# Performance work log

Measured on AMD Instinct MI355X. Metric: run time of the kernel, lower is better.

## Reference

```python
import jax, jax.numpy as jnp
import numpy as np

B, OUT, IN = 128, 1024, 1024
MASK_DENSITY = 0.05  # ~51 connected variable nodes per check node


def setup_inputs() -> dict:
    key = jax.random.key(0)
    kx, km = jax.random.split(key)
    x = jax.random.normal(kx, (B, IN), dtype=jnp.float32)
    # sparse binary connectivity mask [out_features, in_features]
    layer_mask = (jax.random.uniform(km, (OUT, IN)) < MASK_DENSITY).astype(jnp.float32)
    return {"x": x, "layer_mask": layer_mask}


def reference(x, layer_mask):
    # x: [B, IN], layer_mask: [OUT, IN]
    # Vectorized form of: for each output i, product over nonzero entries of
    # x * layer_mask[i]; zero if the masked row is entirely zero.
    xm = x[:, None, :] * layer_mask[None, :, :]          # [B, OUT, IN]
    nz = xm != 0                                          # [B, OUT, IN]
    prod = jnp.prod(jnp.where(nz, xm, jnp.ones_like(xm)), axis=-1)  # [B, OUT]
    return jnp.where(nz.any(axis=-1), prod, jnp.zeros_like(prod))    # [B, OUT]
```

## Files before the change

### kernel.cpp

```cpp
#include <hip/hip_runtime.h>

#define B_SZ   128
#define OUT_SZ 1024
#define IN_SZ  1024
#define IDX_STRIDE 1024


__global__ __launch_bounds__(512) void prep(const float* __restrict__ x,
                                            const float* __restrict__ mask,
                                            float* __restrict__ xT,
                                            int* __restrict__ g_cnt,
                                            int* __restrict__ g_idx) {
    __shared__ int   s_idx[IN_SZ];
    __shared__ int   s_wsum[8];
    __shared__ float s_tile[32][33];

    const int t = threadIdx.x;

    if (blockIdx.x >= OUT_SZ) {
        const int tb = blockIdx.x - OUT_SZ;
        const int c0 = (tb & 31) * 32;
        const int r0 = (tb >> 5) * 32;
        const int tx = t & 31, ty = t >> 5;
#pragma unroll
        for (int j = ty; j < 32; j += 16)
            s_tile[j][tx] = x[(r0 + j) * IN_SZ + c0 + tx];
        __syncthreads();
#pragma unroll
        for (int j = ty; j < 32; j += 16)
            xT[(c0 + j) * B_SZ + r0 + tx] = s_tile[tx][j];
        return;
    }

    const int o    = blockIdx.x;
    const int lane = t & 63;
    const int wv   = t >> 6;

    const float2 m = *reinterpret_cast<const float2*>(mask + o * IN_SZ + t * 2);
    const bool nx = (m.x != 0.0f);
    const bool ny = (m.y != 0.0f);
    const unsigned long long bx = __ballot(nx);
    const unsigned long long by = __ballot(ny);
    const unsigned long long mlow = ((unsigned long long)1 << lane) - 1;
    int off = __popcll(bx & mlow) + __popcll(by & mlow);
    if (lane == 0) s_wsum[wv] = __popcll(bx) + __popcll(by);
    __syncthreads();

    int base = 0, cnt = 0;
#pragma unroll
    for (int i = 0; i < 8; ++i) {
        int v = s_wsum[i];
        if (i < wv) base += v;
        cnt += v;
    }
    off += base;
    if (nx) s_idx[off]      = t * 2;
    if (ny) s_idx[off + nx] = t * 2 + 1;
    __syncthreads();

    for (int k = t; k < cnt; k += 512) g_idx[o * IDX_STRIDE + k] = s_idx[k];
    if (t == 0) g_cnt[o] = cnt;
}

__global__ __launch_bounds__(512) void cn_gather(const float* __restrict__ xT,
                                                 const int* __restrict__ g_cnt,
                                                 const int* __restrict__ g_idx,
                                                 float* __restrict__ out) {
    __shared__ int   s_idx[IDX_STRIDE];
    __shared__ float s_part[4][B_SZ];
    __shared__ int   s_nz[4][B_SZ];

    const int o = blockIdx.x;
    const int t = threadIdx.x;
    const int cnt = g_cnt[o];

    for (int k = t; k < cnt; k += 512) s_idx[k] = g_idx[o * IDX_STRIDE + k];
    __syncthreads();

    const int b = t & 127;
    const int s = t >> 7;

    float p0 = 1.0f, p1 = 1.0f;
    int   a0 = 0,    a1 = 0;
    int k = s;
    for (; k + 4 < cnt; k += 8) {
        const float v0 = xT[s_idx[k]     * B_SZ + b];
        const float v1 = xT[s_idx[k + 4] * B_SZ + b];
        const bool n0 = (v0 != 0.0f), n1 = (v1 != 0.0f);
        p0 *= n0 ? v0 : 1.0f;  a0 |= n0;
        p1 *= n1 ? v1 : 1.0f;  a1 |= n1;
    }
    if (k < cnt) {
        const float v0 = xT[s_idx[k] * B_SZ + b];
        const bool n0 = (v0 != 0.0f);
        p0 *= n0 ? v0 : 1.0f;  a0 |= n0;
    }
    s_part[s][b] = p0 * p1;
    s_nz[s][b]   = a0 | a1;
    __syncthreads();

    if (t < B_SZ) {
        const float p = s_part[0][t] * s_part[1][t] * s_part[2][t] * s_part[3][t];
        const int   a = s_nz[0][t] | s_nz[1][t] | s_nz[2][t] | s_nz[3][t];
        out[t * OUT_SZ + o] = a ? p : 0.0f;
    }
}

extern "C" void kernel_launch(void* const* d_in, const int* in_sizes, int n_in,
                              void* d_out, int out_size, void* d_ws, size_t ws_size,
                              hipStream_t stream) {
    const float* x    = (const float*)d_in[0];
    const float* mask = (const float*)d_in[1];
    float*       out  = (float*)d_out;

    char* ws = (char*)d_ws;
    float* xT    = (float*)(ws);
    int*   g_cnt = (int*)(ws + (512 << 10));
    int*   g_idx = (int*)(ws + (1 << 20));

    prep<<<OUT_SZ + 128, 512, 0, stream>>>(x, mask, xT, g_cnt, g_idx);
    cn_gather<<<OUT_SZ, 512, 0, stream>>>(xT, g_cnt, g_idx, out);
}
```

Measured before the change: 15.43 us.

## Process two outputs per block with float4 gathers in cn_gather

Each cn_gather block now handles two output columns instead of one, halving the grid. Each thread loads a float4 covering four batch entries, and the 16 slices stride over the connected indices. A final reduce over 16 partials per output packs the nonzero flags into a 4-bit mask. The aim is fewer, wider gather instructions and more work per block, at the cost of fewer blocks for parallelism and a longer serial reduction over 16 partials.

```diff
diff --git a/kernel.cpp b/kernel.cpp
--- a/kernel.cpp
+++ b/kernel.cpp
@@ -4,6 +4,7 @@
 #define OUT_SZ 1024
 #define IN_SZ  1024
 #define IDX_STRIDE 1024
+#define OPB    2
 
 
 __global__ __launch_bounds__(512) void prep(const float* __restrict__ x,
@@ -66,43 +67,57 @@
                                                  const int* __restrict__ g_cnt,
                                                  const int* __restrict__ g_idx,
                                                  float* __restrict__ out) {
-    __shared__ int   s_idx[IDX_STRIDE];
-    __shared__ float s_part[4][B_SZ];
-    __shared__ int   s_nz[4][B_SZ];
+    __shared__ int    s_idx[OPB][IDX_STRIDE];
+    __shared__ float4 s_part[OPB][16][32];
+    __shared__ int    s_nzm[OPB][16][32];
 
-    const int o = blockIdx.x;
-    const int t = threadIdx.x;
-    const int cnt = g_cnt[o];
+    const int o0 = blockIdx.x * OPB;
+    const int t  = threadIdx.x;
 
-    for (int k = t; k < cnt; k += 512) s_idx[k] = g_idx[o * IDX_STRIDE + k];
+    int cnt[OPB];
+#pragma unroll
+    for (int j = 0; j < OPB; ++j) {
+        cnt[j] = g_cnt[o0 + j];
+        for (int k = t; k < cnt[j]; k += 512)
+            s_idx[j][k] = g_idx[(o0 + j) * IDX_STRIDE + k];
+    }
     __syncthreads();
 
-    const int b = t & 127;
-    const int s = t >> 7;
+    const int bg = t & 31;
+    const int s  = t >> 5;
+    const float4* xT4 = reinterpret_cast<const float4*>(xT);
 
-    float p0 = 1.0f, p1 = 1.0f;
-    int   a0 = 0,    a1 = 0;
-    int k = s;
-    for (; k + 4 < cnt; k += 8) {
-        const float v0 = xT[s_idx[k]     * B_SZ + b];
-        const float v1 = xT[s_idx[k + 4] * B_SZ + b];
-        const bool n0 = (v0 != 0.0f), n1 = (v1 != 0.0f);
-        p0 *= n0 ? v0 : 1.0f;  a0 |= n0;
-        p1 *= n1 ? v1 : 1.0f;  a1 |= n1;
+#pragma unroll
+    for (int j = 0; j < OPB; ++j) {
+        float px = 1.f, py = 1.f, pz = 1.f, pw = 1.f;
+        int m = 0;
+        for (int k = s; k < cnt[j]; k += 16) {
+            const float4 v = xT4[s_idx[j][k] * 32 + bg];
+            const bool ax = (v.x != 0.0f), ay = (v.y != 0.0f);
+            const bool az = (v.z != 0.0f), aw = (v.w != 0.0f);
+            px *= ax ? v.x : 1.f;  py *= ay ? v.y : 1.f;
+            pz *= az ? v.z : 1.f;  pw *= aw ? v.w : 1.f;
+            m |= (ax ? 1 : 0) | (ay ? 2 : 0) | (az ? 4 : 0) | (aw ? 8 : 0);
+        }
+        s_part[j][s][bg] = make_float4(px, py, pz, pw);
+        s_nzm[j][s][bg]  = m;
     }
-    if (k < cnt) {
-        const float v0 = xT[s_idx[k] * B_SZ + b];
-        const bool n0 = (v0 != 0.0f);
-        p0 *= n0 ? v0 : 1.0f;  a0 |= n0;
-    }
-    s_part[s][b] = p0 * p1;
-    s_nz[s][b]   = a0 | a1;
     __syncthreads();
 
-    if (t < B_SZ) {
-        const float p = s_part[0][t] * s_part[1][t] * s_part[2][t] * s_part[3][t];
-        const int   a = s_nz[0][t] | s_nz[1][t] | s_nz[2][t] | s_nz[3][t];
-        out[t * OUT_SZ + o] = a ? p : 0.0f;
+    if (t < B_SZ * OPB) {
+        const int b = t >> 1;
+        const int j = t & 1;
+        const float* sp = reinterpret_cast<const float*>(&s_part[j][0][0]);
+        const int*   sm = &s_nzm[j][0][0];
+        const int bg2 = b >> 2, c = b & 3;
+        float p = 1.f;
+        int   m = 0;
+#pragma unroll
+        for (int s2 = 0; s2 < 16; ++s2) {
+            p *= sp[s2 * 128 + b];
+            m |= sm[s2 * 32 + bg2];
+        }
+        out[b * OUT_SZ + o0 + j] = ((m >> c) & 1) ? p : 0.0f;
     }
 }
 
@@ -119,5 +134,5 @@
     int*   g_idx = (int*)(ws + (1 << 20));
 
     prep<<<OUT_SZ + 128, 512, 0, stream>>>(x, mask, xT, g_cnt, g_idx);
-    cn_gather<<<OUT_SZ, 512, 0, stream>>>(xT, g_cnt, g_idx, out);
+    cn_gather<<<OUT_SZ / OPB, 512, 0, stream>>>(xT, g_cnt, g_idx, out);
 }
```

Result: no change. 15.56 us (+0.8%).
